# Performance work log

Measured on AMD Instinct MI355X. Metric: run time of the kernel, lower is better.

Reference implementation:

```python
import jax, jax.numpy as jnp
import numpy as np

B, TOK, D, H, L = 64, 20, 512, 8, 4
S = 512          # tokens per half
HD = D // H
ODIM = 32        # encoder_output_dim


def _ln(x, g, b):
    m = x.mean(-1, keepdims=True)
    v = ((x - m) ** 2).mean(-1, keepdims=True)
    return (x - m) / jnp.sqrt(v + 1e-5) * g + b


def _alibi_slopes(h):
    # mirrors FlashAttentionBlock.build_alibi_slopes (base=2.0)
    base = 2.0
    return jnp.asarray([1.0 / base ** (i // (h // base)) for i in range(h)], dtype=jnp.float32)


def setup_inputs() -> dict:
    key = jax.random.key(0)
    ks = jax.random.split(key, 16)
    r = lambda i, shape, s=0.02: jax.random.normal(ks[i], shape, jnp.float32) * s
    return {
        'x': jax.random.normal(ks[0], (B, 2 * S * TOK), jnp.float32),
        'in_W': r(1, (TOK, D)), 'in_b': jnp.zeros((D,)),
        'qkv_W': r(2, (L, D, 3 * D)), 'qkv_b': jnp.zeros((L, 3 * D)),
        'ln1_g': jnp.ones((L, D)), 'ln1_b': jnp.zeros((L, D)),
        'ffn_W1': r(3, (L, D, 4 * D)), 'ffn_b1': jnp.zeros((L, 4 * D)),
        'ffn_W2': r(4, (L, 4 * D, D)), 'ffn_b2': jnp.zeros((L, D)),
        'ln2_g': jnp.ones((L, D)), 'ln2_b': jnp.zeros((L, D)),
        'out_W': r(5, (D, ODIM)), 'out_b': jnp.zeros((ODIM,)),
        'd1_W': r(6, (2 * S * ODIM, 256)), 'd1_b': jnp.zeros((256,)),
        'bn1_g': jnp.ones((256,)), 'bn1_b': jnp.zeros((256,)),
        'bn1_m': jnp.zeros((256,)), 'bn1_v': jnp.ones((256,)),
        'd2_W': r(7, (256, 128)), 'd2_b': jnp.zeros((128,)),
        'bn2_g': jnp.ones((128,)), 'bn2_b': jnp.zeros((128,)),
        'bn2_m': jnp.zeros((128,)), 'bn2_v': jnp.ones((128,)),
        'fin_W': r(8, (128, 1)), 'fin_b': jnp.zeros((1,)),
    }


def _forward(x, in_W, in_b, qkv_W, qkv_b, ln1_g, ln1_b, ffn_W1, ffn_b1,
             ffn_W2, ffn_b2, ln2_g, ln2_b, out_W, out_b,
             d1_W, d1_b, bn1_g, bn1_b, bn1_m, bn1_v,
             d2_W, d2_b, bn2_g, bn2_b, bn2_m, bn2_v, fin_W, fin_b):
    slopes = _alibi_slopes(H)                                   # [H]
    pos = jnp.arange(S)
    # non-causal ALiBi bias: -slope * |i - j|, shape [H, S, S]
    bias = -slopes[:, None, None] * jnp.abs(pos[:, None] - pos[None, :]).astype(jnp.float32)
    scale = 1.0 / np.sqrt(HD).astype(np.float32)

    def encode(xh):
        b = xh.shape[0]
        t = xh.reshape(b, S, TOK) @ in_W + in_b                 # [b, S, D]
        for l in range(L):
            res = t
            qkv = (t @ qkv_W[l] + qkv_b[l]).reshape(b, S, 3, H, HD)
            q, k, v = qkv[:, :, 0], qkv[:, :, 1], qkv[:, :, 2]  # [b, S, H, HD]
            scores = jnp.einsum('bqhd,bkhd->bhqk', q, k) * scale + bias[None]
            attn = jax.nn.softmax(scores, axis=-1)
            o = jnp.einsum('bhqk,bkhd->bqhd', attn, v).reshape(b, S, D)
            t = _ln(res + o, ln1_g[l], ln1_b[l])
            res = t
            f = jax.nn.relu(t @ ffn_W1[l] + ffn_b1[l]) @ ffn_W2[l] + ffn_b2[l]
            t = _ln(res + f, ln2_g[l], ln2_b[l])
        return (t @ out_W + out_b).reshape(b, -1)               # [b, S*ODIM]

    half = S * TOK
    h = jnp.concatenate([encode(x[:, :half]), encode(x[:, half:])], axis=-1)
    bn = lambda z, g, bb, m, v: (z - m) / jnp.sqrt(v + 1e-5) * g + bb
    h = bn(jax.nn.relu(h @ d1_W + d1_b), bn1_g, bn1_b, bn1_m, bn1_v)
    h = bn(jax.nn.relu(h @ d2_W + d2_b), bn2_g, bn2_b, bn2_m, bn2_v)
    return (h @ fin_W + fin_b).squeeze(-1)                      # [B]


def reference(x, in_W, in_b, qkv_W, qkv_b, ln1_g, ln1_b, ffn_W1, ffn_b1,
              ffn_W2, ffn_b2, ln2_g, ln2_b, out_W, out_b,
              d1_W, d1_b, bn1_g, bn1_b, bn1_m, bn1_v,
              d2_W, d2_b, bn2_g, bn2_b, bn2_m, bn2_v, fin_W, fin_b):
    return _forward(x, in_W, in_b, qkv_W, qkv_b, ln1_g, ln1_b, ffn_W1, ffn_b1,
                    ffn_W2, ffn_b2, ln2_g, ln2_b, out_W, out_b,
                    d1_W, d1_b, bn1_g, bn1_b, bn1_m, bn1_v,
                    d2_W, d2_b, bn2_g, bn2_b, bn2_m, bn2_v, fin_W, fin_b)
```

## Files before the change

### kernel.cpp

```cpp
#include <hip/hip_runtime.h>

#define DEV __device__ __forceinline__

using bf16x8 = __attribute__((ext_vector_type(8))) __bf16;
using f32x4  = __attribute__((ext_vector_type(4))) float;
using u16x8  = __attribute__((ext_vector_type(8))) unsigned short;
using u16x4  = __attribute__((ext_vector_type(4))) unsigned short;

DEV unsigned short f2bf(float f) {
  unsigned u = __builtin_bit_cast(unsigned, f);
  u += 0x7fffu + ((u >> 16) & 1u);
  return (unsigned short)(u >> 16);
}
DEV float bf2f(unsigned short h) {
  unsigned u = ((unsigned)h) << 16;
  return __builtin_bit_cast(float, u);
}
DEV f32x4 mfma16(u16x8 a, u16x8 b, f32x4 c) {
  return __builtin_amdgcn_mfma_f32_16x16x32_bf16(
      __builtin_bit_cast(bf16x8, a), __builtin_bit_cast(bf16x8, b), c, 0, 0, 0);
}
DEV f32x4 zero4() { f32x4 z = {0.f, 0.f, 0.f, 0.f}; return z; }

DEV void glds16(const unsigned short* g, unsigned short* l) {
  __builtin_amdgcn_global_load_lds(
      (const __attribute__((address_space(1))) unsigned int*)g,
      (__attribute__((address_space(3))) unsigned int*)l, 16, 0, 0);
}

#define PH_BAR()                          \
  do {                                    \
    __builtin_amdgcn_sched_barrier(0);    \
    __builtin_amdgcn_s_barrier();         \
    __builtin_amdgcn_sched_barrier(0);    \
  } while (0)

enum { EPI_BIAS = 0, EPI_RELU = 1, EPI_QKV = 3 };

template <int EPI>
__global__ __launch_bounds__(512, 1) void gemm8p_k(
    const unsigned short* __restrict__ A, const unsigned short* __restrict__ Bt,
    const float* __restrict__ bias, unsigned short* __restrict__ C,
    unsigned short* __restrict__ Cv, int N, int K) {
  __shared__ unsigned short As[2][16384];
  __shared__ unsigned short Bs[2][16384];
  const int tid = threadIdx.x;
  const int lane = tid & 63, wv = tid >> 6;
  const int q = lane >> 4, ln = lane & 15;
  const int wr = wv >> 2, wc = wv & 3;
  const int ln7 = ln & 7;

  const int Nt = gridDim.x, Mt = gridDim.y;
  const int lin = blockIdx.x + Nt * blockIdx.y;
  const int xcd = lin & 7;
  const int j = lin >> 3;
  const int mi = xcd * (Mt >> 3) + j / Nt;
  const int ni = j % Nt;
  const int m0 = mi << 8, n0 = ni << 8;

  f32x4 acc[8][4];
#pragma unroll
  for (int i = 0; i < 8; ++i)
#pragma unroll
    for (int jj = 0; jj < 4; ++jj) acc[i][jj] = zero4();

  const int sr = lane >> 3;
  const int sc = ((lane & 7) ^ sr) << 3;
  const unsigned short* Abase = A + (size_t)(m0 + wv * 8 + sr) * K + sc;
  const unsigned short* Bbase = Bt + (size_t)(n0 + wv * 8 + sr) * K + sc;

  const int T = K >> 6;

  auto stA = [&](int buf, int t, int half) {
    unsigned short* d = &As[buf][(half * 128 + wv * 8) * 64];
    const unsigned short* s = Abase + (size_t)(half * 128) * K + t * 64;
    glds16(s, d);
    glds16(s + (size_t)64 * K, d + 4096);
  };
  auto stB = [&](int buf, int t, int half) {
    unsigned short* d = &Bs[buf][(half * 128 + wv * 8) * 64];
    const unsigned short* s = Bbase + (size_t)(half * 128) * K + t * 64;
    glds16(s, d);
    glds16(s + (size_t)64 * K, d + 4096);
  };

  stB(0, 0, 0);
  stB(0, 0, 1);
  stA(0, 0, 0);
  stA(0, 0, 1);
  if (T > 1) {
    stB(1, 1, 0);
    stB(1, 1, 1);
    asm volatile("s_waitcnt vmcnt(4)" ::: "memory");
  } else {
    asm volatile("s_waitcnt vmcnt(0)" ::: "memory");
  }
  PH_BAR();

  for (int u = 0; u < T; ++u) {
    const int cur = u & 1, nxt = cur ^ 1;
    const unsigned short* Ab = &As[cur][0];
    const unsigned short* Bb = &Bs[cur][0];
    u16x8 a0[4][2], a1[4][2], b0[2][2], b1[2][2];

#pragma unroll
    for (int mt = 0; mt < 4; ++mt)
#pragma unroll
      for (int kk = 0; kk < 2; ++kk)
        a0[mt][kk] = *(const u16x8*)(Ab + (wr * 128 + mt * 16 + ln) * 64 +
                                     (((kk * 4 + q) ^ ln7) << 3));
#pragma unroll
    for (int nt = 0; nt < 2; ++nt)
#pragma unroll
      for (int kk = 0; kk < 2; ++kk)
        b0[nt][kk] = *(const u16x8*)(Bb + (wc * 64 + nt * 16 + ln) * 64 +
                                     (((kk * 4 + q) ^ ln7) << 3));
    if (u + 1 < T) stA(nxt, u + 1, 0);
    PH_BAR();
    __builtin_amdgcn_s_setprio(1);
#pragma unroll
    for (int kk = 0; kk < 2; ++kk)
#pragma unroll
      for (int nt = 0; nt < 2; ++nt)
#pragma unroll
        for (int mt = 0; mt < 4; ++mt)
          acc[mt][nt] = mfma16(a0[mt][kk], b0[nt][kk], acc[mt][nt]);
    __builtin_amdgcn_s_setprio(0);
    PH_BAR();

#pragma unroll
    for (int nt = 0; nt < 2; ++nt)
#pragma unroll
      for (int kk = 0; kk < 2; ++kk)
        b1[nt][kk] = *(const u16x8*)(Bb + (wc * 64 + (nt + 2) * 16 + ln) * 64 +
                                     (((kk * 4 + q) ^ ln7) << 3));
    if (u + 1 < T) stA(nxt, u + 1, 1);
    PH_BAR();
    __builtin_amdgcn_s_setprio(1);
#pragma unroll
    for (int kk = 0; kk < 2; ++kk)
#pragma unroll
      for (int nt = 0; nt < 2; ++nt)
#pragma unroll
        for (int mt = 0; mt < 4; ++mt)
          acc[mt][nt + 2] = mfma16(a0[mt][kk], b1[nt][kk], acc[mt][nt + 2]);
    __builtin_amdgcn_s_setprio(0);
    PH_BAR();

#pragma unroll
    for (int mt = 0; mt < 4; ++mt)
#pragma unroll
      for (int kk = 0; kk < 2; ++kk)
        a1[mt][kk] = *(const u16x8*)(Ab + (wr * 128 + (mt + 4) * 16 + ln) * 64 +
                                     (((kk * 4 + q) ^ ln7) << 3));
    if (u + 2 < T) stB(cur, u + 2, 0);
    PH_BAR();
    __builtin_amdgcn_s_setprio(1);
#pragma unroll
    for (int kk = 0; kk < 2; ++kk)
#pragma unroll
      for (int nt = 0; nt < 2; ++nt)
#pragma unroll
        for (int mt = 0; mt < 4; ++mt)
          acc[mt + 4][nt] = mfma16(a1[mt][kk], b0[nt][kk], acc[mt + 4][nt]);
    __builtin_amdgcn_s_setprio(0);
    PH_BAR();

    if (u + 2 < T) stB(cur, u + 2, 1);
    PH_BAR();
    __builtin_amdgcn_s_setprio(1);
#pragma unroll
    for (int kk = 0; kk < 2; ++kk)
#pragma unroll
      for (int nt = 0; nt < 2; ++nt)
#pragma unroll
        for (int mt = 0; mt < 4; ++mt)
          acc[mt + 4][nt + 2] = mfma16(a1[mt][kk], b1[nt][kk], acc[mt + 4][nt + 2]);
    __builtin_amdgcn_s_setprio(0);
    if (u + 1 < T) {
      if (u + 2 < T) {
        asm volatile("s_waitcnt vmcnt(4)" ::: "memory");
      } else {
        asm volatile("s_waitcnt vmcnt(0)" ::: "memory");
      }
      PH_BAR();
    }
  }

#pragma unroll
  for (int mt = 0; mt < 8; ++mt) {
    const int rowb = m0 + wr * 128 + mt * 16 + q * 4;
    const int seq = rowb >> 9, key0 = rowb & 511;
#pragma unroll
    for (int nt = 0; nt < 4; ++nt) {
      const int col = n0 + wc * 64 + nt * 16 + ln;
      const float bs = bias[col];
      if (EPI == EPI_QKV && n0 >= 1024) {
        const int hh = (col - 1024) >> 6, hd = col & 63;
        u16x4 pk;
#pragma unroll
        for (int r = 0; r < 4; ++r) pk[r] = f2bf(acc[mt][nt][r] + bs);
        *(u16x4*)(Cv + ((size_t)((seq * 8 + hh) * 64 + hd)) * 512 + key0) = pk;
      } else {
#pragma unroll
        for (int r = 0; r < 4; ++r) {
          float v = acc[mt][nt][r] + bs;
          if (EPI == EPI_RELU) v = fmaxf(v, 0.f);
          C[(size_t)(rowb + r) * N + col] = f2bf(v);
        }
      }
    }
  }
}

__global__ __launch_bounds__(256) void outp_k(
    const unsigned short* __restrict__ A, const unsigned short* __restrict__ Bt,
    const float* __restrict__ bias, unsigned short* __restrict__ C) {
  __shared__ unsigned short Asb[256 * 32];
  __shared__ unsigned short Bsb[32 * 520];
  const int tid = threadIdx.x;
  const int lane = tid & 63, wv = tid >> 6;
  const int q = lane >> 4, ln = lane & 15;
  const int m0 = blockIdx.x << 8;
  const int sw = ((q ^ ((ln >> 1) & 3)) << 3);

  {
    const int br = tid >> 3, bc = (tid & 7) * 64;
    const unsigned short* src = Bt + (size_t)br * 512 + bc;
#pragma unroll
    for (int i = 0; i < 8; ++i)
      *(u16x8*)(Bsb + br * 520 + bc + i * 8) = *(const u16x8*)(src + i * 8);
  }

  f32x4 acc[4][2];
#pragma unroll
  for (int i = 0; i < 4; ++i)
#pragma unroll
    for (int jj = 0; jj < 2; ++jj) acc[i][jj] = zero4();

  const int sr = lane >> 2;
  const int sc = ((lane & 3) ^ ((lane >> 3) & 3)) << 3;
  const unsigned short* Ap = A + (size_t)(m0 + wv * 64 + sr) * 512 + sc;
  unsigned short* AsW = Asb + (wv * 64) * 32;

  for (int kb = 0; kb < 512; kb += 32) {
    __syncthreads();
    glds16(Ap + kb, AsW);
    glds16(Ap + (size_t)16 * 512 + kb, AsW + 512);
    glds16(Ap + (size_t)32 * 512 + kb, AsW + 1024);
    glds16(Ap + (size_t)48 * 512 + kb, AsW + 1536);
    __syncthreads();
    u16x8 af[4];
#pragma unroll
    for (int mt = 0; mt < 4; ++mt)
      af[mt] = *(const u16x8*)(Asb + (wv * 64 + mt * 16 + ln) * 32 + sw);
#pragma unroll
    for (int nt = 0; nt < 2; ++nt) {
      u16x8 bf = *(const u16x8*)(Bsb + (nt * 16 + ln) * 520 + kb + q * 8);
#pragma unroll
      for (int mt = 0; mt < 4; ++mt) acc[mt][nt] = mfma16(af[mt], bf, acc[mt][nt]);
    }
  }

#pragma unroll
  for (int mt = 0; mt < 4; ++mt) {
    const int rowb = m0 + wv * 64 + mt * 16 + q * 4;
#pragma unroll
    for (int nt = 0; nt < 2; ++nt) {
      const int col = nt * 16 + ln;
      const float bs = bias[col];
#pragma unroll
      for (int r = 0; r < 4; ++r)
        C[(size_t)(rowb + r) * 32 + col] = f2bf(acc[mt][nt][r] + bs);
    }
  }
}

__global__ __launch_bounds__(256) void attn_k(const unsigned short* __restrict__ qkv,
                                              const unsigned short* __restrict__ vt,
                                              unsigned short* __restrict__ o) {
  __shared__ unsigned short Qs[128 * 72];
  __shared__ unsigned short Ks[2][64 * 64];
  __shared__ unsigned short Vts[2][64 * 64];
  unsigned short* Ps = Qs;
  const int tid = threadIdx.x;
  const int lane = tid & 63, w = tid >> 6, q = lane >> 4, ln = lane & 15;
  const int bh = blockIdx.x;
  const int seq = bh >> 3, h = bh & 7;
  const int qt = blockIdx.y;
  const size_t tokb = (size_t)seq * 512;
  const int qoff = h * 64, koff = 512 + h * 64;
  const float c1 = 0.125f * 1.44269504f;
  const float c2 = ((h < 4) ? 1.0f : 0.5f) * 1.44269504f;

#pragma unroll
  for (int p = 0; p < 4; ++p) {
    int c = p * 256 + tid;
    int row = c >> 3, cc = (c & 7) << 3;
    u16x8 v = *(const u16x8*)(qkv + (tokb + qt * 128 + row) * 1536 + qoff + cc);
    *(u16x8*)(Qs + row * 72 + cc) = v;
  }

  const int sr = lane >> 3;
  const int sc = ((lane & 7) ^ sr) << 3;
  const unsigned short* Kp = qkv + (tokb + w * 16 + sr) * 1536 + koff + sc;
  const unsigned short* Vp = vt + ((size_t)bh * 64 + w * 16 + sr) * 512 + sc;
  const int ln7 = ln & 7;

  auto stage = [&](int kt, int buf) {
    unsigned short* KsW = &Ks[buf][w * 1024];
    unsigned short* VsW = &Vts[buf][w * 1024];
    glds16(Kp + (size_t)(kt * 64) * 1536, KsW);
    glds16(Kp + (size_t)(kt * 64 + 8) * 1536, KsW + 512);
    glds16(Vp + kt * 64, VsW);
    glds16(Vp + kt * 64 + (size_t)8 * 512, VsW + 512);
  };

  stage(0, 0);

  __syncthreads();
  u16x8 aq[2][2];
#pragma unroll
  for (int mt = 0; mt < 2; ++mt)
#pragma unroll
    for (int kc = 0; kc < 2; ++kc)
      aq[mt][kc] = *(const u16x8*)(Qs + (w * 32 + mt * 16 + ln) * 72 + kc * 32 + q * 8);

  float lacc[2] = {0.f, 0.f};
  f32x4 o_acc[2][4];
#pragma unroll
  for (int mt = 0; mt < 2; ++mt)
#pragma unroll
    for (int ht = 0; ht < 4; ++ht) o_acc[mt][ht] = zero4();

  for (int kt = 0; kt < 8; ++kt) {
    const int buf = kt & 1;
    __syncthreads();
    if (kt + 1 < 8) {
      stage(kt + 1, buf ^ 1);
      asm volatile("s_waitcnt vmcnt(4)" ::: "memory");
    } else {
      asm volatile("s_waitcnt vmcnt(0)" ::: "memory");
    }
    __builtin_amdgcn_sched_barrier(0);
    __builtin_amdgcn_s_barrier();
    __builtin_amdgcn_sched_barrier(0);

    f32x4 sacc[2][4];
#pragma unroll
    for (int mt = 0; mt < 2; ++mt)
#pragma unroll
      for (int nt = 0; nt < 4; ++nt) sacc[mt][nt] = zero4();
#pragma unroll
    for (int nt = 0; nt < 4; ++nt)
#pragma unroll
      for (int kc = 0; kc < 2; ++kc) {
        u16x8 bk = *(const u16x8*)(&Ks[buf][(nt * 16 + ln) * 64 + (((kc * 4 + q) ^ ln7) << 3)]);
#pragma unroll
        for (int mt = 0; mt < 2; ++mt) sacc[mt][nt] = mfma16(bk, aq[mt][kc], sacc[mt][nt]);
      }

    const float qp0 = (float)(qt * 128 + w * 32 + ln);
    const float kb0 = (float)(kt * 64 + q * 4);
#pragma unroll
    for (int mt = 0; mt < 2; ++mt) {
      const float qpm = qp0 + (float)(mt * 16);
#pragma unroll
      for (int nt = 0; nt < 4; ++nt) {
        const float kp = kb0 + (float)(nt * 16);
        u16x4 pk;
#pragma unroll
        for (int r = 0; r < 4; ++r) {
          const float ad = fabsf(qpm - (kp + (float)r));
          const float p = exp2f(fmaf(sacc[mt][nt][r], c1, -c2 * ad));
          const unsigned u = __builtin_bit_cast(unsigned, p);
          const unsigned short pb = (unsigned short)((u + 0x8000u) >> 16);
          pk[r] = pb;
          lacc[mt] += bf2f(pb);
        }
        *(u16x4*)(Ps + (w * 32 + mt * 16 + ln) * 72 + nt * 16 + q * 4) = pk;
      }
    }
#pragma unroll
    for (int kc = 0; kc < 2; ++kc) {
      u16x8 pa[2];
#pragma unroll
      for (int mt = 0; mt < 2; ++mt)
        pa[mt] = *(const u16x8*)(Ps + (w * 32 + mt * 16 + ln) * 72 + kc * 32 + q * 8);
#pragma unroll
      for (int ht = 0; ht < 4; ++ht) {
        u16x8 bv = *(const u16x8*)(&Vts[buf][(ht * 16 + ln) * 64 + (((kc * 4 + q) ^ ln7) << 3)]);
#pragma unroll
        for (int mt = 0; mt < 2; ++mt) o_acc[mt][ht] = mfma16(pa[mt], bv, o_acc[mt][ht]);
      }
    }
  }

  float rl[2][4];
#pragma unroll
  for (int mt = 0; mt < 2; ++mt) {
    float l = lacc[mt];
    l += __shfl_xor(l, 16, 64);
    l += __shfl_xor(l, 32, 64);
    const int sb = (lane >> 4) * 20;
#pragma unroll
    for (int r = 0; r < 4; ++r) rl[mt][r] = 1.0f / __shfl(l, sb + r, 64);
  }

#pragma unroll
  for (int mt = 0; mt < 2; ++mt)
#pragma unroll
    for (int ht = 0; ht < 4; ++ht)
#pragma unroll
      for (int r = 0; r < 4; ++r) {
        const int row = qt * 128 + w * 32 + mt * 16 + q * 4 + r;
        const float val = o_acc[mt][ht][r] * rl[mt][r];
        o[(tokb + row) * 512 + h * 64 + ht * 16 + ln] = f2bf(val);
      }
}

__global__ __launch_bounds__(256) void ln_k(const unsigned short* res,
                                            const unsigned short* __restrict__ y,
                                            const float* __restrict__ g,
                                            const float* __restrict__ b,
                                            unsigned short* out) {
  const int lane = threadIdx.x & 63, wv = threadIdx.x >> 6;
  const size_t row = (size_t)blockIdx.x * 4 + wv;
  const size_t base = row * 512 + lane * 8;
  u16x8 rv = *(const u16x8*)(res + base);
  u16x8 yv = *(const u16x8*)(y + base);
  float v[8];
  float s = 0.f, s2 = 0.f;
#pragma unroll
  for (int i = 0; i < 8; ++i) {
    v[i] = bf2f(rv[i]) + bf2f(yv[i]);
    s += v[i];
    s2 += v[i] * v[i];
  }
#pragma unroll
  for (int m = 1; m < 64; m <<= 1) {
    s += __shfl_xor(s, m, 64);
    s2 += __shfl_xor(s2, m, 64);
  }
  const float mean = s * (1.f / 512.f);
  const float var = s2 * (1.f / 512.f) - mean * mean;
  const float rstd = rsqrtf(var + 1e-5f);
  const int c = lane * 8;
  u16x8 ov;
#pragma unroll
  for (int i = 0; i < 8; ++i) ov[i] = f2bf((v[i] - mean) * rstd * g[c + i] + b[c + i]);
  *(u16x8*)(out + base) = ov;
}

__global__ __launch_bounds__(256) void transpose_w(const float* __restrict__ in,
                                                   unsigned short* __restrict__ out,
                                                   int Kin, int Nin, int Kout, int Nout) {
  __shared__ float tile[32][33];
  const int nb = blockIdx.x * 32, kb = blockIdx.y * 32;
  const int tx = threadIdx.x & 31, ty = threadIdx.x >> 5;
#pragma unroll
  for (int i = 0; i < 32; i += 8) {
    int k = kb + ty + i, n = nb + tx;
    tile[ty + i][tx] = (k < Kin && n < Nin) ? in[(size_t)k * Nin + n] : 0.f;
  }
  __syncthreads();
#pragma unroll
  for (int i = 0; i < 32; i += 8) {
    int n = nb + ty + i, k = kb + tx;
    if (n < Nout && k < Kout) out[(size_t)n * Kout + k] = f2bf(tile[tx][ty + i]);
  }
}

__global__ __launch_bounds__(256) void xpad_k(const float* __restrict__ x,
                                              unsigned short* __restrict__ xp) {
  const int idx = blockIdx.x * 256 + threadIdx.x;
  const int tok = idx >> 6, k = idx & 63;
  const int seq = tok >> 9, s = tok & 511;
  const int hf = seq >> 6, b = seq & 63;
  float v = 0.f;
  if (k < 20) v = x[(size_t)b * 20480 + hf * 10240 + s * 20 + k];
  xp[idx] = f2bf(v);
}

__global__ __launch_bounds__(256) void d1_part(const unsigned short* __restrict__ enc,
                                               const float* __restrict__ W,
                                               float* __restrict__ pz) {
  __shared__ float ef[64 * 128];
  const int tid = threadIdx.x;
  const int kb = blockIdx.x * 128;
  const int hf = kb >> 14;
  const int j0 = kb & 16383;
  {
    const int m = tid >> 2, c = (tid & 3) * 32;
    const unsigned short* src = enc + (size_t)hf * 1048576 + (size_t)m * 16384 + j0 + c;
#pragma unroll
    for (int i = 0; i < 4; ++i) {
      u16x8 v = *(const u16x8*)(src + i * 8);
#pragma unroll
      for (int jj = 0; jj < 8; ++jj) ef[m * 128 + c + i * 8 + jj] = bf2f(v[jj]);
    }
  }
  __syncthreads();
  const int n = tid;
  float acc[64];
#pragma unroll
  for (int m = 0; m < 64; ++m) acc[m] = 0.f;
  for (int kc = 0; kc < 128; kc += 4) {
    const float w0 = W[(size_t)(kb + kc) * 256 + n];
    const float w1 = W[(size_t)(kb + kc + 1) * 256 + n];
    const float w2 = W[(size_t)(kb + kc + 2) * 256 + n];
    const float w3 = W[(size_t)(kb + kc + 3) * 256 + n];
#pragma unroll
    for (int m = 0; m < 64; ++m) {
      const f32x4 e = *(const f32x4*)(ef + m * 128 + kc);
      acc[m] += e[0] * w0 + e[1] * w1 + e[2] * w2 + e[3] * w3;
    }
  }
#pragma unroll
  for (int m = 0; m < 64; ++m)
    pz[(size_t)(blockIdx.x * 64 + m) * 256 + n] = acc[m];
}

__global__ __launch_bounds__(256) void d1_fin(const float* __restrict__ pz,
                                              const float* __restrict__ d1b,
                                              const float* __restrict__ g,
                                              const float* __restrict__ b,
                                              const float* __restrict__ mm,
                                              const float* __restrict__ vv,
                                              float* __restrict__ h1) {
  const int m = blockIdx.x, n = threadIdx.x;
  float a = d1b[n];
  for (int sl = 0; sl < 256; ++sl) a += pz[(size_t)(sl * 64 + m) * 256 + n];
  a = fmaxf(a, 0.f);
  a = (a - mm[n]) * rsqrtf(vv[n] + 1e-5f) * g[n] + b[n];
  h1[m * 256 + n] = a;
}

__global__ __launch_bounds__(128) void d2_k(const float* __restrict__ h1,
                                            const float* __restrict__ W,
                                            const float* __restrict__ bb,
                                            const float* __restrict__ g,
                                            const float* __restrict__ b,
                                            const float* __restrict__ mm,
                                            const float* __restrict__ vv,
                                            float* __restrict__ h2) {
  __shared__ float hs[256];
  const int m = blockIdx.x, n = threadIdx.x;
  hs[n] = h1[m * 256 + n];
  hs[n + 128] = h1[m * 256 + n + 128];
  __syncthreads();
  float a = bb[n];
#pragma unroll 8
  for (int k = 0; k < 256; ++k) a += hs[k] * W[k * 128 + n];
  a = fmaxf(a, 0.f);
  a = (a - mm[n]) * rsqrtf(vv[n] + 1e-5f) * g[n] + b[n];
  h2[m * 128 + n] = a;
}

__global__ __launch_bounds__(64) void fin_k(const float* __restrict__ h2,
                                            const float* __restrict__ W,
                                            const float* __restrict__ fb,
                                            float* __restrict__ out) {
  const int m = threadIdx.x;
  float a = fb[0];
#pragma unroll 8
  for (int k = 0; k < 128; ++k) a += h2[m * 128 + k] * W[k];
  out[m] = a;
}

extern "C" void kernel_launch(void* const* d_in, const int* in_sizes, int n_in,
                              void* d_out, int out_size, void* d_ws, size_t ws_size,
                              hipStream_t stream) {
  const float* x      = (const float*)d_in[0];
  const float* in_W   = (const float*)d_in[1];
  const float* in_b   = (const float*)d_in[2];
  const float* qkv_W  = (const float*)d_in[3];
  const float* qkv_b  = (const float*)d_in[4];
  const float* ln1_g  = (const float*)d_in[5];
  const float* ln1_b  = (const float*)d_in[6];
  const float* ffn_W1 = (const float*)d_in[7];
  const float* ffn_b1 = (const float*)d_in[8];
  const float* ffn_W2 = (const float*)d_in[9];
  const float* ffn_b2 = (const float*)d_in[10];
  const float* ln2_g  = (const float*)d_in[11];
  const float* ln2_b  = (const float*)d_in[12];
  const float* out_W  = (const float*)d_in[13];
  const float* out_b  = (const float*)d_in[14];
  const float* d1W    = (const float*)d_in[15];
  const float* d1b    = (const float*)d_in[16];
  const float* bn1g   = (const float*)d_in[17];
  const float* bn1b   = (const float*)d_in[18];
  const float* bn1m   = (const float*)d_in[19];
  const float* bn1v   = (const float*)d_in[20];
  const float* d2W    = (const float*)d_in[21];
  const float* d2b    = (const float*)d_in[22];
  const float* bn2g   = (const float*)d_in[23];
  const float* bn2b   = (const float*)d_in[24];
  const float* bn2m   = (const float*)d_in[25];
  const float* bn2v   = (const float*)d_in[26];
  const float* finW   = (const float*)d_in[27];
  const float* finb   = (const float*)d_in[28];
  (void)in_sizes; (void)n_in; (void)out_size; (void)ws_size;

  char* ws = (char*)d_ws;
  size_t off = 0;
  auto alloc = [&](size_t bytes) {
    char* p = ws + off;
    off += (bytes + 255) & ~(size_t)255;
    return p;
  };
  unsigned short* t     = (unsigned short*)alloc(32768ull * 512 * 2);
  unsigned short* big   = (unsigned short*)alloc(32768ull * 2048 * 2);
  unsigned short* ob    = (unsigned short*)alloc(32768ull * 512 * 2);
  unsigned short* xpad  = (unsigned short*)alloc(65536ull * 64 * 2);
  unsigned short* enc   = (unsigned short*)alloc(65536ull * 32 * 2);
  unsigned short* inWt  = (unsigned short*)alloc(512ull * 64 * 2);
  unsigned short* qkvWt = (unsigned short*)alloc(4ull * 1536 * 512 * 2);
  unsigned short* f1Wt  = (unsigned short*)alloc(4ull * 2048 * 512 * 2);
  unsigned short* f2Wt  = (unsigned short*)alloc(4ull * 512 * 2048 * 2);
  unsigned short* outWt = (unsigned short*)alloc(128ull * 512 * 2);
  float* h1 = (float*)alloc(64ull * 256 * 4);
  float* h2 = (float*)alloc(64ull * 128 * 4);
  float* pz = (float*)big;
  unsigned short* vtb = big + (size_t)32768 * 1536;

  xpad_k<<<16384, 256, 0, stream>>>(x, xpad);
  transpose_w<<<dim3(16, 2), 256, 0, stream>>>(in_W, inWt, 20, 512, 64, 512);
  transpose_w<<<dim3(4, 16), 256, 0, stream>>>(out_W, outWt, 512, 32, 512, 128);
  for (int l = 0; l < 4; ++l) {
    transpose_w<<<dim3(48, 16), 256, 0, stream>>>(qkv_W + (size_t)l * 512 * 1536,
                                                  qkvWt + (size_t)l * 1536 * 512, 512, 1536, 512, 1536);
    transpose_w<<<dim3(64, 16), 256, 0, stream>>>(ffn_W1 + (size_t)l * 512 * 2048,
                                                  f1Wt + (size_t)l * 2048 * 512, 512, 2048, 512, 2048);
    transpose_w<<<dim3(16, 64), 256, 0, stream>>>(ffn_W2 + (size_t)l * 2048 * 512,
                                                  f2Wt + (size_t)l * 512 * 2048, 2048, 512, 2048, 512);
  }

  for (int hf = 0; hf < 2; ++hf) {
    gemm8p_k<EPI_BIAS><<<dim3(2, 128), 512, 0, stream>>>(xpad + (size_t)hf * 32768 * 64, inWt, in_b, t, nullptr, 512, 64);
    for (int l = 0; l < 4; ++l) {
      gemm8p_k<EPI_QKV><<<dim3(6, 128), 512, 0, stream>>>(t, qkvWt + (size_t)l * 1536 * 512,
                                                          qkv_b + l * 1536, big, vtb, 1536, 512);
      attn_k<<<dim3(512, 4), 256, 0, stream>>>(big, vtb, ob);
      ln_k<<<8192, 256, 0, stream>>>(t, ob, ln1_g + l * 512, ln1_b + l * 512, t);
      gemm8p_k<EPI_RELU><<<dim3(8, 128), 512, 0, stream>>>(t, f1Wt + (size_t)l * 2048 * 512,
                                                           ffn_b1 + l * 2048, big, nullptr, 2048, 512);
      gemm8p_k<EPI_BIAS><<<dim3(2, 128), 512, 0, stream>>>(big, f2Wt + (size_t)l * 512 * 2048,
                                                           ffn_b2 + l * 512, ob, nullptr, 512, 2048);
      ln_k<<<8192, 256, 0, stream>>>(t, ob, ln2_g + l * 512, ln2_b + l * 512, t);
    }
    outp_k<<<128, 256, 0, stream>>>(t, outWt, out_b, enc + (size_t)hf * 32768 * 32);
  }

  d1_part<<<256, 256, 0, stream>>>(enc, d1W, pz);
  d1_fin<<<64, 256, 0, stream>>>(pz, d1b, bn1g, bn1b, bn1m, bn1v, h1);
  d2_k<<<64, 128, 0, stream>>>(h1, d2W, d2b, bn2g, bn2b, bn2m, bn2v, h2);
  fin_k<<<1, 64, 0, stream>>>(h2, finW, finb, (float*)d_out);
}
```

Before: 2.933 ms.

## Make GEMM blocks loop over several N tiles with cross-tile prefetch

The GEMM kernel gains an NTILES template parameter, so each block now walks several consecutive 256-wide N tiles in one flattened loop. The QKV GEMM launches 256 blocks of 3 tiles and the FFN1 GEMM 256 blocks of 4 tiles, instead of one block per tile. The double-buffered global-to-LDS prefetch carries on across tile boundaries, and each finished tile's epilogue is written out inside the loop. The aim is to cut block launch and prologue/drain overhead and keep the pipeline full between tiles. In exchange the epilogue stores now sit inside the main loop and can stall it, and the A tile is still reloaded for every N tile.

```diff
diff --git a/kernel.cpp b/kernel.cpp
--- a/kernel.cpp
+++ b/kernel.cpp
@@ -37,7 +37,7 @@
 
 enum { EPI_BIAS = 0, EPI_RELU = 1, EPI_QKV = 3 };
 
-template <int EPI>
+template <int EPI, int NTILES>
 __global__ __launch_bounds__(512, 1) void gemm8p_k(
     const unsigned short* __restrict__ A, const unsigned short* __restrict__ Bt,
     const float* __restrict__ bias, unsigned short* __restrict__ C,
@@ -55,8 +55,9 @@
   const int xcd = lin & 7;
   const int j = lin >> 3;
   const int mi = xcd * (Mt >> 3) + j / Nt;
-  const int ni = j % Nt;
-  const int m0 = mi << 8, n0 = ni << 8;
+  const int gi = j % Nt;
+  const int m0 = mi << 8;
+  const int gbase = gi * NTILES;
 
   f32x4 acc[8][4];
 #pragma unroll
@@ -67,9 +68,10 @@
   const int sr = lane >> 3;
   const int sc = ((lane & 7) ^ sr) << 3;
   const unsigned short* Abase = A + (size_t)(m0 + wv * 8 + sr) * K + sc;
-  const unsigned short* Bbase = Bt + (size_t)(n0 + wv * 8 + sr) * K + sc;
+  const unsigned short* Bgrp = Bt + (size_t)(gbase * 256 + wv * 8 + sr) * K + sc;
 
   const int T = K >> 6;
+  const int V = T * NTILES;
 
   auto stA = [&](int buf, int t, int half) {
     unsigned short* d = &As[buf][(half * 128 + wv * 8) * 64];
@@ -77,28 +79,69 @@
     glds16(s, d);
     glds16(s + (size_t)64 * K, d + 4096);
   };
-  auto stB = [&](int buf, int t, int half) {
+  auto stB = [&](int buf, int niw, int t, int half) {
     unsigned short* d = &Bs[buf][(half * 128 + wv * 8) * 64];
-    const unsigned short* s = Bbase + (size_t)(half * 128) * K + t * 64;
+    const unsigned short* s = Bgrp + (size_t)(niw * 256 + half * 128) * K + t * 64;
     glds16(s, d);
     glds16(s + (size_t)64 * K, d + 4096);
   };
 
-  stB(0, 0, 0);
-  stB(0, 0, 1);
+  auto writeC = [&](int n0w) {
+#pragma unroll
+    for (int mt = 0; mt < 8; ++mt) {
+      const int rowb = m0 + wr * 128 + mt * 16 + q * 4;
+      const int seq = rowb >> 9, key0 = rowb & 511;
+#pragma unroll
+      for (int nt = 0; nt < 4; ++nt) {
+        const int col = n0w + wc * 64 + nt * 16 + ln;
+        const float bs = bias[col];
+        if (EPI == EPI_QKV && n0w >= 1024) {
+          const int hh = (col - 1024) >> 6, hd = col & 63;
+          u16x4 pk;
+#pragma unroll
+          for (int r = 0; r < 4; ++r) pk[r] = f2bf(acc[mt][nt][r] + bs);
+          *(u16x4*)(Cv + ((size_t)((seq * 8 + hh) * 64 + hd)) * 512 + key0) = pk;
+        } else {
+#pragma unroll
+          for (int r = 0; r < 4; ++r) {
+            float v = acc[mt][nt][r] + bs;
+            if (EPI == EPI_RELU) v = fmaxf(v, 0.f);
+            C[(size_t)(rowb + r) * N + col] = f2bf(v);
+          }
+        }
+      }
+    }
+#pragma unroll
+    for (int i = 0; i < 8; ++i)
+#pragma unroll
+      for (int jj = 0; jj < 4; ++jj) acc[i][jj] = zero4();
+  };
+
+  stB(0, 0, 0, 0);
+  stB(0, 0, 0, 1);
   stA(0, 0, 0);
   stA(0, 0, 1);
-  if (T > 1) {
-    stB(1, 1, 0);
-    stB(1, 1, 1);
+  if (V > 1) {
+    const int n1p = (T == 1) ? 1 : 0, t1p = (T == 1) ? 0 : 1;
+    stB(1, n1p, t1p, 0);
+    stB(1, n1p, t1p, 1);
     asm volatile("s_waitcnt vmcnt(4)" ::: "memory");
   } else {
     asm volatile("s_waitcnt vmcnt(0)" ::: "memory");
   }
   PH_BAR();
 
-  for (int u = 0; u < T; ++u) {
-    const int cur = u & 1, nxt = cur ^ 1;
+  int t = 0, niw = 0;
+  for (int v = 0; v < V; ++v) {
+    const int cur = v & 1, nxt = cur ^ 1;
+    int t1 = t + 1, n1 = niw;
+    if (t1 == T) { t1 = 0; ++n1; }
+    int t2 = t1 + 1, n2 = n1;
+    if (t2 == T) { t2 = 0; ++n2; }
+    const bool h1 = (v + 1 < V), h2 = (v + 2 < V);
+
+    if (t == 0 && v > 0) writeC((gbase + niw - 1) << 8);
+
     const unsigned short* Ab = &As[cur][0];
     const unsigned short* Bb = &Bs[cur][0];
     u16x8 a0[4][2], a1[4][2], b0[2][2], b1[2][2];
@@ -115,7 +158,7 @@
       for (int kk = 0; kk < 2; ++kk)
         b0[nt][kk] = *(const u16x8*)(Bb + (wc * 64 + nt * 16 + ln) * 64 +
                                      (((kk * 4 + q) ^ ln7) << 3));
-    if (u + 1 < T) stA(nxt, u + 1, 0);
+    if (h1) stA(nxt, t1, 0);
     PH_BAR();
     __builtin_amdgcn_s_setprio(1);
 #pragma unroll
@@ -134,7 +177,7 @@
       for (int kk = 0; kk < 2; ++kk)
         b1[nt][kk] = *(const u16x8*)(Bb + (wc * 64 + (nt + 2) * 16 + ln) * 64 +
                                      (((kk * 4 + q) ^ ln7) << 3));
-    if (u + 1 < T) stA(nxt, u + 1, 1);
+    if (h1) stA(nxt, t1, 1);
     PH_BAR();
     __builtin_amdgcn_s_setprio(1);
 #pragma unroll
@@ -153,7 +196,7 @@
       for (int kk = 0; kk < 2; ++kk)
         a1[mt][kk] = *(const u16x8*)(Ab + (wr * 128 + (mt + 4) * 16 + ln) * 64 +
                                      (((kk * 4 + q) ^ ln7) << 3));
-    if (u + 2 < T) stB(cur, u + 2, 0);
+    if (h2) stB(cur, n2, t2, 0);
     PH_BAR();
     __builtin_amdgcn_s_setprio(1);
 #pragma unroll
@@ -166,7 +209,7 @@
     __builtin_amdgcn_s_setprio(0);
     PH_BAR();
 
-    if (u + 2 < T) stB(cur, u + 2, 1);
+    if (h2) stB(cur, n2, t2, 1);
     PH_BAR();
     __builtin_amdgcn_s_setprio(1);
 #pragma unroll
@@ -177,40 +220,20 @@
         for (int mt = 0; mt < 4; ++mt)
           acc[mt + 4][nt + 2] = mfma16(a1[mt][kk], b1[nt][kk], acc[mt + 4][nt + 2]);
     __builtin_amdgcn_s_setprio(0);
-    if (u + 1 < T) {
-      if (u + 2 < T) {
+    if (h1) {
+      if (h2) {
         asm volatile("s_waitcnt vmcnt(4)" ::: "memory");
       } else {
         asm volatile("s_waitcnt vmcnt(0)" ::: "memory");
       }
       PH_BAR();
     }
-  }
-
-#pragma unroll
-  for (int mt = 0; mt < 8; ++mt) {
-    const int rowb = m0 + wr * 128 + mt * 16 + q * 4;
-    const int seq = rowb >> 9, key0 = rowb & 511;
-#pragma unroll
-    for (int nt = 0; nt < 4; ++nt) {
-      const int col = n0 + wc * 64 + nt * 16 + ln;
-      const float bs = bias[col];
-      if (EPI == EPI_QKV && n0 >= 1024) {
-        const int hh = (col - 1024) >> 6, hd = col & 63;
-        u16x4 pk;
-#pragma unroll
-        for (int r = 0; r < 4; ++r) pk[r] = f2bf(acc[mt][nt][r] + bs);
-        *(u16x4*)(Cv + ((size_t)((seq * 8 + hh) * 64 + hd)) * 512 + key0) = pk;
-      } else {
-#pragma unroll
-        for (int r = 0; r < 4; ++r) {
-          float v = acc[mt][nt][r] + bs;
-          if (EPI == EPI_RELU) v = fmaxf(v, 0.f);
-          C[(size_t)(rowb + r) * N + col] = f2bf(v);
-        }
-      }
-    }
-  }
+
+    ++t;
+    if (t == T) { t = 0; ++niw; }
+  }
+
+  writeC((gbase + NTILES - 1) << 8);
 }
 
 __global__ __launch_bounds__(256) void outp_k(
@@ -637,16 +660,17 @@
   }
 
   for (int hf = 0; hf < 2; ++hf) {
-    gemm8p_k<EPI_BIAS><<<dim3(2, 128), 512, 0, stream>>>(xpad + (size_t)hf * 32768 * 64, inWt, in_b, t, nullptr, 512, 64);
+    gemm8p_k<EPI_BIAS, 1><<<dim3(2, 128), 512, 0, stream>>>(
+        xpad + (size_t)hf * 32768 * 64, inWt, in_b, t, nullptr, 512, 64);
     for (int l = 0; l < 4; ++l) {
-      gemm8p_k<EPI_QKV><<<dim3(6, 128), 512, 0, stream>>>(t, qkvWt + (size_t)l * 1536 * 512,
-                                                          qkv_b + l * 1536, big, vtb, 1536, 512);
+      gemm8p_k<EPI_QKV, 3><<<dim3(2, 128), 512, 0, stream>>>(
+          t, qkvWt + (size_t)l * 1536 * 512, qkv_b + l * 1536, big, vtb, 1536, 512);
       attn_k<<<dim3(512, 4), 256, 0, stream>>>(big, vtb, ob);
       ln_k<<<8192, 256, 0, stream>>>(t, ob, ln1_g + l * 512, ln1_b + l * 512, t);
-      gemm8p_k<EPI_RELU><<<dim3(8, 128), 512, 0, stream>>>(t, f1Wt + (size_t)l * 2048 * 512,
-                                                           ffn_b1 + l * 2048, big, nullptr, 2048, 512);
-      gemm8p_k<EPI_BIAS><<<dim3(2, 128), 512, 0, stream>>>(big, f2Wt + (size_t)l * 512 * 2048,
-                                                           ffn_b2 + l * 512, ob, nullptr, 512, 2048);
+      gemm8p_k<EPI_RELU, 4><<<dim3(2, 128), 512, 0, stream>>>(
+          t, f1Wt + (size_t)l * 2048 * 512, ffn_b1 + l * 2048, big, nullptr, 2048, 512);
+      gemm8p_k<EPI_BIAS, 1><<<dim3(2, 128), 512, 0, stream>>>(
+          big, f2Wt + (size_t)l * 512 * 2048, ffn_b2 + l * 512, ob, nullptr, 512, 2048);
       ln_k<<<8192, 256, 0, stream>>>(t, ob, ln2_g + l * 512, ln2_b + l * 512, t);
     }
     outp_k<<<128, 256, 0, stream>>>(t, outWt, out_b, enc + (size_t)hf * 32768 * 32);
```

Measured after the change: 3.446 ms. 1.17x slower.
